# Kernel tuning notes

Hardware: AMD Instinct MI355X
Metric: run time of the kernel (lower is better)

## Reference

```python
import jax, jax.numpy as jnp
import numpy as np
from jax import lax

# L segments, N candidate spans per segment, S words per segment,
# MAX_W max span width, K spans kept, D_EMB = 3*768 span emb, D_HID ffnn hidden
L, N, S, MAX_W, K, D_EMB, D_HID = 8, 7168, 256, 30, 128, 2304, 150


def setup_inputs():
    key = jax.random.key(0)
    k0, k1, k2, k3, k4 = jax.random.split(key, 5)
    span_emb = jax.random.normal(k0, (L, N, D_EMB), dtype=jnp.float32)
    W1 = jax.random.normal(k1, (D_EMB, D_HID), dtype=jnp.float32) * 0.02
    b1 = jnp.zeros((D_HID,), jnp.float32)
    W2 = jax.random.normal(k2, (D_HID, 1), dtype=jnp.float32) * 0.02
    b2 = jnp.zeros((1,), jnp.float32)
    starts = jax.random.randint(k3, (L, N), 0, S - MAX_W, dtype=jnp.int32)
    widths = jax.random.randint(k4, (L, N), 0, MAX_W, dtype=jnp.int32)
    ends = starts + widths  # valid spans: start <= end < S, width < MAX_W
    return {"span_emb": span_emb, "W1": W1, "b1": b1, "W2": W2, "b2": b2,
            "candidate_starts": starts, "candidate_ends": ends,
            "num_output_spans": K, "max_sentence_length": S}


def _extract_one(scores, starts, ends, k_out, max_len):
    """Greedy non-crossing span selection for one segment (ExtractSpans, sort_spans=True).

    latest_end[j]   = latest end among selected spans starting at j   (init -1)
    earliest_start[j] = earliest start among selected spans ending at j (init +inf)
    A candidate (s,e) crosses a selected span iff exists j in (s,e] with
    latest_end[j] > e, or j in [s,e) with earliest_start[j] < s.
    """
    pad = max_len + MAX_W + 1
    order = jnp.argsort(-scores).astype(jnp.int32)  # descending by score
    s_srt, e_srt = starts[order], ends[order]
    offs = jnp.arange(MAX_W + 1, dtype=jnp.int32)

    def step(carry, xs):
        le, es, sel, n = carry
        i, s, e = xs
        win_le = lax.dynamic_slice(le, (s,), (MAX_W + 1,))  # j = s .. s+MAX_W
        win_es = lax.dynamic_slice(es, (s,), (MAX_W + 1,))
        w = e - s
        crossing = jnp.any((offs >= 1) & (offs <= w) & (win_le > e)) | \
                   jnp.any((offs < w) & (win_es < s))
        take = jnp.logical_and(~crossing, n < k_out)
        nc = jnp.minimum(n, k_out - 1)
        sel = sel.at[nc].set(jnp.where(take, i, sel[nc]))
        le = le.at[s].set(jnp.where(take, jnp.maximum(le[s], e), le[s]))
        es = es.at[e].set(jnp.where(take, jnp.minimum(es[e], s), es[e]))
        return (le, es, sel, n + take.astype(jnp.int32)), None

    init = (jnp.full((pad,), -1, jnp.int32),
            jnp.full((pad,), pad, jnp.int32),
            jnp.zeros((k_out,), jnp.int32),
            jnp.int32(0))
    (le, es, sel, n), _ = lax.scan(step, init, (order, s_srt, e_srt))

    # sort_spans=True: reorder selected spans by (start, end); pad tail with first.
    slot = jnp.arange(k_out, dtype=jnp.int32)
    sortkey = jnp.where(slot < n, starts[sel] * pad + ends[sel], jnp.int32(2**31 - 1))
    sel_sorted = sel[jnp.argsort(sortkey)]
    return jnp.where(slot < n, sel_sorted, sel_sorted[0])


def reference(span_emb, W1, b1, W2, b2, candidate_starts, candidate_ends,
              num_output_spans, max_sentence_length):
    # FFNN mention scoring (ffnn_m: Linear -> ReLU -> Linear, output size 1)
    h = jax.nn.relu(jnp.einsum('lnd,dh->lnh', span_emb, W1) + b1)
    scores = (jnp.einsum('lnh,ho->lno', h, W2) + b2)[..., 0]  # [L, N]
    idx = jax.vmap(lambda sc, st, en: _extract_one(sc, st, en,
                                                   num_output_spans,
                                                   max_sentence_length))(
        scores, candidate_starts, candidate_ends)  # [L, K] int32
    sel_scores = jnp.take_along_axis(scores, idx, axis=1)  # [L, K]
    return sel_scores, idx
```

## Files before the change

kernel.cpp:

```cpp
#include <hip/hip_runtime.h>
#include <stdint.h>

#define LSEG 8
#define NCAND 7168
#define SLEN 256
#define MAXW 30
#define KOUT 128
#define DEMB 2304
#define DHID 150
#define PADV (SLEN + MAXW + 1)

#define MTILE 112
#define NPAD 160
#define KT 32

typedef const unsigned int __attribute__((address_space(1)))* gp_t;
typedef unsigned int __attribute__((address_space(3)))* lp_t;

__device__ __forceinline__ void gload16(const float* g, float* l) {
    __builtin_amdgcn_global_load_lds((gp_t)g, (lp_t)l, 16, 0, 0);
}

__global__ __launch_bounds__(256) void k_transpose(const float* __restrict__ w1,
                                                   float* __restrict__ w1t) {
    int i = blockIdx.x * 256 + threadIdx.x;
    if (i < DHID * DEMB) {
        int n = i / DEMB;
        int k = i - n * DEMB;
        w1t[i] = w1[k * DHID + n];
    }
}

__global__ __launch_bounds__(256, 2) void k_scores(
    const float* __restrict__ emb, const float* __restrict__ w1t,
    const float* __restrict__ b1, const float* __restrict__ w2,
    const float* __restrict__ b2, float* __restrict__ scores) {
    __shared__ float smem[(MTILE + NPAD) * KT];
    float* amem = smem;
    float* wmem = smem + MTILE * KT;

    const int tid = threadIdx.x;
    const int tx = tid & 15;
    const int ty = tid >> 4;
    const int M0 = blockIdx.x * MTILE;

    for (int u = tid; u < (NPAD - DHID) * KT; u += 256) wmem[DHID * KT + u] = 0.f;

    float acc[7][10];
#pragma unroll
    for (int i = 0; i < 7; ++i)
#pragma unroll
        for (int j = 0; j < 10; ++j) acc[i][j] = 0.f;

    for (int k0 = 0; k0 < DEMB; k0 += KT) {
#pragma unroll
        for (int r = 0; r < 4; ++r) {
            int u = tid + 256 * r;
            if (u < MTILE * 8) {
                int row = u >> 3, cd = u & 7;
                int gc = cd ^ (row & 7);
                gload16(emb + (size_t)(M0 + row) * DEMB + k0 + gc * 4, amem + u * 4);
            }
        }
#pragma unroll
        for (int r = 0; r < 5; ++r) {
            int u = tid + 256 * r;
            if (u < DHID * 8) {
                int row = u >> 3, cd = u & 7;
                int gc = cd ^ (row & 7);
                gload16(w1t + (size_t)row * DEMB + k0 + gc * 4, wmem + u * 4);
            }
        }
        __syncthreads();

#pragma unroll 2
        for (int kc = 0; kc < 8; ++kc) {
            float4 av[7];
            float4 wv[10];
#pragma unroll
            for (int i = 0; i < 7; ++i) {
                int row = ty * 7 + i;
                av[i] = *(const float4*)(amem + row * KT + ((kc ^ (row & 7)) << 2));
            }
#pragma unroll
            for (int j = 0; j < 10; ++j) {
                int n = tx + 16 * j;
                wv[j] = *(const float4*)(wmem + n * KT + ((kc ^ (tx & 7)) << 2));
            }
#pragma unroll
            for (int i = 0; i < 7; ++i) {
#pragma unroll
                for (int j = 0; j < 10; ++j) {
                    acc[i][j] += av[i].x * wv[j].x;
                    acc[i][j] += av[i].y * wv[j].y;
                    acc[i][j] += av[i].z * wv[j].z;
                    acc[i][j] += av[i].w * wv[j].w;
                }
            }
        }
        __syncthreads();
    }

    float partial[7];
#pragma unroll
    for (int i = 0; i < 7; ++i) partial[i] = 0.f;
#pragma unroll
    for (int j = 0; j < 10; ++j) {
        int n = tx + 16 * j;
        float bb = (n < DHID) ? b1[n] : 0.f;
        float ww = (n < DHID) ? w2[n] : 0.f;
#pragma unroll
        for (int i = 0; i < 7; ++i) {
            float h = acc[i][j] + bb;
            h = fmaxf(h, 0.f);
            partial[i] += h * ww;
        }
    }
    float* red = smem;
#pragma unroll
    for (int i = 0; i < 7; ++i) red[(ty * 7 + i) * 17 + tx] = partial[i];
    __syncthreads();
    if (tid < MTILE) {
        float sacc = 0.f;
#pragma unroll
        for (int t = 0; t < 16; ++t) sacc += red[tid * 17 + t];
        scores[M0 + tid] = sacc + b2[0];
    }
}

__global__ __launch_bounds__(1024) void k_extract(
    const float* __restrict__ scores,
    const int* __restrict__ cs, const int* __restrict__ ce,
    float* __restrict__ out_sc, float* __restrict__ out_idx) {
    __shared__ unsigned ks[8192];
    __shared__ unsigned short id[8192];
    __shared__ int le[352];
    __shared__ int es[352];
    __shared__ int sel_idx[KOUT];
    __shared__ unsigned sel_se[KOUT];
    __shared__ unsigned skey[KOUT];
    __shared__ int nshare;

    const int tid = threadIdx.x;
    const int l = blockIdx.x;
    const int base = l * NCAND;

    for (int i = tid; i < 352; i += 1024) { le[i] = -1; es[i] = PADV; }
    if (tid < KOUT) { sel_idx[tid] = 0; sel_se[tid] = 0; }

    for (int t = tid; t < 8192; t += 1024) {
        if (t < NCAND) {
            unsigned u = __float_as_uint(scores[base + t]);
            u = (u & 0x80000000u) ? ~u : (u | 0x80000000u);
            ks[t] = ~u;
            id[t] = (unsigned short)t;
        } else {
            ks[t] = 0xFFFFFFFFu;
            id[t] = 0xFFFFu;
        }
    }

    for (int k = 2; k <= 8192; k <<= 1) {
        for (int j = k >> 1; j > 0; j >>= 1) {
            __syncthreads();
            for (int t = tid; t < 8192; t += 1024) {
                int p = t ^ j;
                if (p > t) {
                    unsigned ka = ks[t], kb = ks[p];
                    unsigned short ia = id[t], ib = id[p];
                    bool agtb = (ka > kb) || (ka == kb && ia > ib);
                    bool up = ((t & k) == 0);
                    if (agtb == up) {
                        ks[t] = kb; ks[p] = ka;
                        id[t] = ib; id[p] = ia;
                    }
                }
            }
        }
    }
    __syncthreads();

    for (int t = tid; t < NCAND; t += 1024) {
        int i0 = id[t];
        ks[t] = (unsigned)cs[base + i0] | ((unsigned)ce[base + i0] << 16);
    }
    __syncthreads();

    if (tid < 64) {
        volatile int* lev = le;
        volatile int* esv = es;
        const int lane = tid;
        int n = 0;
        for (int t0 = 0; t0 < NCAND && n < KOUT; t0 += 64) {
            const int t = t0 + lane;
            const unsigned se = ks[t];
            const int s = (int)(se & 0xFFFFu);
            const int e = (int)(se >> 16);
            const int w = e - s;
            bool cr = false;
#pragma unroll
            for (int ro = 0; ro <= MAXW; ++ro) {
                int lv = lev[s + ro];
                int ev = esv[s + ro];
                cr = cr || ((ro >= 1) && (ro <= w) && (lv > e));
                cr = cr || ((ro < w) && (ev < s));
            }
            unsigned long long ok = __ballot(!cr);
            unsigned long long taken = 0ull;
            const int nbase = n;
            while (ok) {
                int j = __builtin_ctzll(ok);
                ok &= ok - 1ull;
                int sj = __shfl(s, j);
                int ej = __shfl(e, j);
                bool crj = (s < sj && sj <= e && e < ej) ||
                           (sj < s && s <= ej && ej < e);
                unsigned long long cm = __ballot(crj);
                if ((cm & taken) == 0ull) {
                    taken |= (1ull << j);
                    ++n;
                    if (n >= KOUT) break;
                }
            }
            if ((taken >> lane) & 1ull) {
                int slot = nbase + __popcll(taken & ((1ull << lane) - 1ull));
                sel_idx[slot] = (int)id[t];
                sel_se[slot] = se;
                atomicMax(&le[s], e);
                atomicMin(&es[e], s);
            }
            __threadfence_block();
        }
        if (lane == 0) nshare = n;
    }
    __syncthreads();

    const int nsel = nshare;
    if (tid < KOUT) {
        if (tid < nsel) {
            unsigned se = sel_se[tid];
            int s = (int)(se & 0xFFFFu);
            int e = (int)(se >> 16);
            skey[tid] = ((unsigned)(s * PADV + e) << 7) | (unsigned)tid;
        } else {
            skey[tid] = 0x7F000000u | (unsigned)tid;
        }
    }
    for (int k = 2; k <= KOUT; k <<= 1) {
        for (int j = k >> 1; j > 0; j >>= 1) {
            __syncthreads();
            if (tid < KOUT) {
                int t = tid, p = t ^ j;
                if (p > t) {
                    unsigned a = skey[t], b = skey[p];
                    bool up = ((t & k) == 0);
                    if ((a > b) == up) { skey[t] = b; skey[p] = a; }
                }
            }
        }
    }
    __syncthreads();
    if (tid < KOUT) {
        int oslot = (int)(skey[tid] & 127u);
        int slot0 = (int)(skey[0] & 127u);
        int oi = (tid < nsel) ? sel_idx[oslot] : sel_idx[slot0];
        out_idx[l * KOUT + tid] = (float)oi;
        out_sc[l * KOUT + tid] = scores[base + oi];
    }
}

extern "C" void kernel_launch(void* const* d_in, const int* in_sizes, int n_in,
                              void* d_out, int out_size, void* d_ws, size_t ws_size,
                              hipStream_t stream) {
    const float* emb = (const float*)d_in[0];
    const float* w1  = (const float*)d_in[1];
    const float* b1  = (const float*)d_in[2];
    const float* w2  = (const float*)d_in[3];
    const float* b2  = (const float*)d_in[4];
    const int*   cs  = (const int*)d_in[5];
    const int*   ce  = (const int*)d_in[6];

    float* ws_scores = (float*)d_ws;
    float* ws_w1t    = (float*)((char*)d_ws + 262144);

    k_transpose<<<dim3(1350), dim3(256), 0, stream>>>(w1, ws_w1t);
    k_scores<<<dim3((LSEG * NCAND) / MTILE), dim3(256), 0, stream>>>(
        emb, ws_w1t, b1, w2, b2, ws_scores);
    k_extract<<<dim3(LSEG), dim3(1024), 0, stream>>>(
        ws_scores, cs, ce, (float*)d_out, (float*)d_out + LSEG * KOUT);
}
```

Before: 1.390 ms.

## Double-buffer GEMM K tiles in LDS and trim selection-loop fences

The scoring GEMM now uses two LDS buffers with a K tile of 16, so the async global-to-LDS loads for the next tile are issued while the current tile is being computed. Load addressing is precomputed per thread and the XOR swizzle is adapted to the narrower tile. In the greedy selection loop the volatile LDS reads become plain reads, and the block fence now runs only when some span was taken in that batch. Risks are fewer K steps of work per sync, and correctness now depends on the remaining fence to keep LDS values visible, since the loads are no longer volatile.

```diff
diff --git a/kernel.cpp b/kernel.cpp
--- a/kernel.cpp
+++ b/kernel.cpp
@@ -12,7 +12,8 @@
 
 #define MTILE 112
 #define NPAD 160
-#define KT 32
+#define KT 16
+#define BUF ((MTILE + NPAD) * KT)
 
 typedef const unsigned int __attribute__((address_space(1)))* gp_t;
 typedef unsigned int __attribute__((address_space(3)))* lp_t;
@@ -35,16 +36,27 @@
     const float* __restrict__ emb, const float* __restrict__ w1t,
     const float* __restrict__ b1, const float* __restrict__ w2,
     const float* __restrict__ b2, float* __restrict__ scores) {
-    __shared__ float smem[(MTILE + NPAD) * KT];
-    float* amem = smem;
-    float* wmem = smem + MTILE * KT;
+    __shared__ float smem[2 * BUF];
 
     const int tid = threadIdx.x;
     const int tx = tid & 15;
     const int ty = tid >> 4;
     const int M0 = blockIdx.x * MTILE;
 
-    for (int u = tid; u < (NPAD - DHID) * KT; u += 256) wmem[DHID * KT + u] = 0.f;
+    const int gc = (tid & 3) ^ ((tid >> 3) & 3);
+    const int arow = tid >> 2;
+    const float* gA0 = emb + (size_t)(M0 + arow) * DEMB + gc * 4;
+    const float* gA1 = gA0 + (size_t)64 * DEMB;
+    const float* gW0 = w1t + (size_t)arow * DEMB + gc * 4;
+    const float* gW1 = gW0 + (size_t)64 * DEMB;
+    const float* gW2 = gW0 + (size_t)128 * DEMB;
+    const bool has_a1 = (tid < 192);
+    const bool has_w2 = (tid < 88);
+
+    if (tid < NPAD) {
+        smem[(MTILE + DHID) * KT + tid] = 0.f;
+        smem[BUF + (MTILE + DHID) * KT + tid] = 0.f;
+    }
 
     float acc[7][10];
 #pragma unroll
@@ -52,40 +64,49 @@
 #pragma unroll
         for (int j = 0; j < 10; ++j) acc[i][j] = 0.f;
 
-    for (int k0 = 0; k0 < DEMB; k0 += KT) {
-#pragma unroll
-        for (int r = 0; r < 4; ++r) {
-            int u = tid + 256 * r;
-            if (u < MTILE * 8) {
-                int row = u >> 3, cd = u & 7;
-                int gc = cd ^ (row & 7);
-                gload16(emb + (size_t)(M0 + row) * DEMB + k0 + gc * 4, amem + u * 4);
-            }
-        }
-#pragma unroll
-        for (int r = 0; r < 5; ++r) {
-            int u = tid + 256 * r;
-            if (u < DHID * 8) {
-                int row = u >> 3, cd = u & 7;
-                int gc = cd ^ (row & 7);
-                gload16(w1t + (size_t)row * DEMB + k0 + gc * 4, wmem + u * 4);
-            }
-        }
-        __syncthreads();
-
-#pragma unroll 2
-        for (int kc = 0; kc < 8; ++kc) {
+    const int NT = DEMB / KT;
+
+    {
+        float* am = smem;
+        float* wm = smem + MTILE * KT;
+        gload16(gA0, am + tid * 4);
+        if (has_a1) gload16(gA1, am + (tid + 256) * 4);
+        gload16(gW0, wm + tid * 4);
+        gload16(gW1, wm + (tid + 256) * 4);
+        if (has_w2) gload16(gW2, wm + (tid + 512) * 4);
+    }
+    __syncthreads();
+
+    const int wsw = (tx >> 1) & 3;
+
+    for (int t = 0; t < NT; ++t) {
+        const int cur = t & 1;
+        if (t + 1 < NT) {
+            float* am = smem + (cur ^ 1) * BUF;
+            float* wm = am + MTILE * KT;
+            const int ko = (t + 1) * KT;
+            gload16(gA0 + ko, am + tid * 4);
+            if (has_a1) gload16(gA1 + ko, am + (tid + 256) * 4);
+            gload16(gW0 + ko, wm + tid * 4);
+            gload16(gW1 + ko, wm + (tid + 256) * 4);
+            if (has_w2) gload16(gW2 + ko, wm + (tid + 512) * 4);
+        }
+        const float* am = smem + cur * BUF;
+        const float* wm = am + MTILE * KT;
+#pragma unroll
+        for (int kc = 0; kc < 4; ++kc) {
             float4 av[7];
             float4 wv[10];
 #pragma unroll
             for (int i = 0; i < 7; ++i) {
                 int row = ty * 7 + i;
-                av[i] = *(const float4*)(amem + row * KT + ((kc ^ (row & 7)) << 2));
+                av[i] = *(const float4*)(am + row * KT +
+                                         ((kc ^ ((row >> 1) & 3)) << 2));
             }
 #pragma unroll
             for (int j = 0; j < 10; ++j) {
                 int n = tx + 16 * j;
-                wv[j] = *(const float4*)(wmem + n * KT + ((kc ^ (tx & 7)) << 2));
+                wv[j] = *(const float4*)(wm + n * KT + ((kc ^ wsw) << 2));
             }
 #pragma unroll
             for (int i = 0; i < 7; ++i) {
@@ -187,8 +208,6 @@
     __syncthreads();
 
     if (tid < 64) {
-        volatile int* lev = le;
-        volatile int* esv = es;
         const int lane = tid;
         int n = 0;
         for (int t0 = 0; t0 < NCAND && n < KOUT; t0 += 64) {
@@ -200,8 +219,8 @@
             bool cr = false;
 #pragma unroll
             for (int ro = 0; ro <= MAXW; ++ro) {
-                int lv = lev[s + ro];
-                int ev = esv[s + ro];
+                int lv = le[s + ro];
+                int ev = es[s + ro];
                 cr = cr || ((ro >= 1) && (ro <= w) && (lv > e));
                 cr = cr || ((ro < w) && (ev < s));
             }
@@ -222,14 +241,16 @@
                     if (n >= KOUT) break;
                 }
             }
-            if ((taken >> lane) & 1ull) {
-                int slot = nbase + __popcll(taken & ((1ull << lane) - 1ull));
-                sel_idx[slot] = (int)id[t];
-                sel_se[slot] = se;
-                atomicMax(&le[s], e);
-                atomicMin(&es[e], s);
-            }
-            __threadfence_block();
+            if (taken) {
+                if ((taken >> lane) & 1ull) {
+                    int slot = nbase + __popcll(taken & ((1ull << lane) - 1ull));
+                    sel_idx[slot] = (int)id[t];
+                    sel_se[slot] = se;
+                    atomicMax(&le[s], e);
+                    atomicMin(&es[e], s);
+                }
+                __threadfence_block();
+            }
         }
         if (lane == 0) nshare = n;
     }
```

After: 1.360 ms. 2.1% less time.
